# Kernel optimization log

Measured on AMD Instinct MI355X. Metric: run time of the kernel, lower is better.

## Reference

```python
import jax, jax.numpy as jnp
import numpy as np

NUM_RBF = 16
K_NB = 30
N_LAYERS = 4
N_HEADS = 4
HID = 64

def _ln(x, g, b, eps=1e-5):
    m = jnp.mean(x, -1, keepdims=True)
    v = jnp.mean((x - m) ** 2, -1, keepdims=True)
    return (x - m) / jnp.sqrt(v + eps) * g + b

def _edges(coords, mask):
    # KNN graph from Calpha coords; RBF-embed neighbor distances.
    mask2d = mask[:, :, None] * mask[:, None, :]                      # [B,L,L]
    dX = coords[:, :, None, :] - coords[:, None, :, :]
    D = jnp.sqrt(jnp.sum(dX * dX, -1) + 1e-6)                         # [B,L,L]
    D_max = jnp.max(D, -1, keepdims=True)
    D_adj = D + (1.0 - mask2d) * D_max                                # push padded pairs far away
    negD, E_idx = jax.lax.top_k(-D_adj, K_NB)                         # k smallest distances
    D_nb = -negD                                                      # [B,L,K]
    mu = jnp.linspace(2.0, 22.0, NUM_RBF)
    sigma = (22.0 - 2.0) / NUM_RBF
    rbf = jnp.exp(-(((D_nb[..., None] - mu) / sigma) ** 2))           # [B,L,K,16]
    return rbf, E_idx

def _gather(h, idx):
    # h [B,L,C], idx [B,L,K] -> [B,L,K,C]
    return jax.vmap(lambda hb, ib: hb[ib])(h, idx)

def setup_inputs() -> dict:
    key = jax.random.key(0)
    ks = iter(jax.random.split(key, 40))
    B, L, F = 8, 2048, 1038
    def w(shape, fan_in):
        return jax.random.normal(next(ks), shape, jnp.float32) / np.sqrt(fan_in)
    return {
        "coords": jax.random.normal(next(ks), (B, L, 3), jnp.float32) * 10.0,
        "node_features": jax.random.normal(next(ks), (B, L, F), jnp.float32),
        "mask": jnp.ones((B, L), jnp.float32),
        "W_node": w((F, HID), F), "b_node": jnp.zeros((HID,), jnp.float32),
        "W_ee": w((NUM_RBF, NUM_RBF), NUM_RBF),
        "g_eln": jnp.ones((NUM_RBF,), jnp.float32), "b_eln": jnp.zeros((NUM_RBF,), jnp.float32),
        "W_ep": w((NUM_RBF, HID), NUM_RBF), "b_ep": jnp.zeros((HID,), jnp.float32),
        "WQ": w((N_LAYERS, HID, HID), HID), "bQ": jnp.zeros((N_LAYERS, HID), jnp.float32),
        "WK": w((N_LAYERS, 2 * HID, HID), 2 * HID), "bK": jnp.zeros((N_LAYERS, HID), jnp.float32),
        "WV": w((N_LAYERS, 2 * HID, HID), 2 * HID), "bV": jnp.zeros((N_LAYERS, HID), jnp.float32),
        "WO": w((N_LAYERS, HID, HID), HID), "bO": jnp.zeros((N_LAYERS, HID), jnp.float32),
        "g1": jnp.ones((N_LAYERS, HID), jnp.float32), "b1": jnp.zeros((N_LAYERS, HID), jnp.float32),
        "W1": w((N_LAYERS, HID, 4 * HID), HID), "bf1": jnp.zeros((N_LAYERS, 4 * HID), jnp.float32),
        "W2": w((N_LAYERS, 4 * HID, HID), 4 * HID), "bf2": jnp.zeros((N_LAYERS, HID), jnp.float32),
        "g2": jnp.ones((N_LAYERS, HID), jnp.float32), "b2": jnp.zeros((N_LAYERS, HID), jnp.float32),
        "W_out": w((HID, 1), HID), "b_out": jnp.zeros((1,), jnp.float32),
    }

def reference(coords, node_features, mask, W_node, b_node, W_ee, g_eln, b_eln,
              W_ep, b_ep, WQ, bQ, WK, bK, WV, bV, WO, bO, g1, b1,
              W1, bf1, W2, bf2, g2, b2, W_out, b_out):
    B, L = mask.shape
    d = HID // N_HEADS
    rbf, E_idx = _edges(coords, mask)
    E = _ln(rbf @ W_ee, g_eln, b_eln)                                 # EdgeFeatures embedding+norm
    h_E = E @ W_ep + b_ep                                             # [B,L,K,HID]
    h_V = node_features @ W_node + b_node                             # [B,L,HID]
    mask_attend = _gather(mask[..., None], E_idx)[..., 0] * mask[..., None]  # [B,L,K]
    for l in range(N_LAYERS):
        h_EV = jnp.concatenate([h_E, _gather(h_V, E_idx)], -1)        # [B,L,K,2*HID]
        Q = (h_V @ WQ[l] + bQ[l]).reshape(B, L, N_HEADS, d)
        Kt = (h_EV @ WK[l] + bK[l]).reshape(B, L, K_NB, N_HEADS, d)
        V = (h_EV @ WV[l] + bV[l]).reshape(B, L, K_NB, N_HEADS, d)
        logits = jnp.einsum('blhd,blkhd->blhk', Q, Kt) / np.sqrt(d).astype(np.float32)
        m = mask_attend[:, :, None, :]                                # [B,L,1,K]
        logits = jnp.where(m > 0, logits, jnp.finfo(logits.dtype).min)
        attend = jax.nn.softmax(logits, -1) * m
        upd = jnp.einsum('blhk,blkhd->blhd', attend, V).reshape(B, L, HID)
        dh = upd @ WO[l] + bO[l]
        h_V = _ln(h_V + dh, g1[l], b1[l])
        ffn = jax.nn.relu(h_V @ W1[l] + bf1[l]) @ W2[l] + bf2[l]
        h_V = _ln(h_V + ffn, g2[l], b2[l])
        h_V = h_V * mask[..., None]
    logits_out = (h_V @ W_out + b_out)[..., 0]                        # [B,L]
    return logits_out
```

## Files before the change

### kernel.cpp

```cpp
#include <hip/hip_runtime.h>
#include <hip/hip_fp16.h>

#define L_ 2048
#define NROW 16384
#define FIN 1038

__global__ __launch_bounds__(256) void k_node_part(const float* __restrict__ X,
                                                   const float* __restrict__ W,
                                                   float* __restrict__ Part) {
  const int rb = blockIdx.x >> 2;
  const int split = blockIdx.x & 3;
  const int kStart = split * 260;
  const int kEnd = (split == 3) ? FIN : (kStart + 260);
  const int t = threadIdx.x;
  const int row0 = rb * 128;
  __shared__ float Xs[2][16][132];
  __shared__ float Ws[2][16][64];
  const int ri = t >> 3;
  const int ci = t & 7;
  const int sxr = t >> 2;
  const int sxk = (t & 3) * 4;
  const int swr = t >> 4;
  const int swc = (t & 15) * 4;

// ... 131 lines not shown
  float dmax = 0.f;
#pragma unroll
  for (int u = 0; u < 8; u++) {
    int j = t + 256 * u;
    float dx = cix - cb[j * 3 + 0];
    float dy = ciy - cb[j * 3 + 1];
    float dz = ciz - cb[j * 3 + 2];
    float dist = sqrtf(dx * dx + dy * dy + dz * dz + 1e-6f);
    d[u] = dist;
    mj[u] = mb[j];
    dmax = fmaxf(dmax, dist);
  }
#pragma unroll
  for (int off = 32; off; off >>= 1) dmax = fmaxf(dmax, __shfl_xor(dmax, off, 64));
  if (lane == 0) sredf[wid] = dmax;
#pragma unroll
  for (int q = 0; q < 8; q++) hist[t * 8 + q] = 0u;
  __syncthreads();
  dmax = fmaxf(fmaxf(sredf[0], sredf[1]), fmaxf(sredf[2], sredf[3]));
  const float scale = 1024.0f / fmaxf(dmax, 1e-20f);
  float adj[8];
  int bin[8];
#pragma unroll
  for (int u = 0; u < 8; u++) {
    adj[u] = d[u] + (1.f - mi * mj[u]) * dmax;
    int bi = (int)(adj[u] * scale);
    bin[u] = bi < 2047 ? bi : 2047;
    atomicAdd(&hist[bin[u]], 1u);
  }
  __syncthreads();
  unsigned int c[8];
  unsigned int local = 0;
#pragma unroll
  for (int q = 0; q < 8; q++) { c[q] = hist[t * 8 + q]; local += c[q]; }
  unsigned int incl = local;
#pragma unroll
  for (int off = 1; off < 64; off <<= 1) {
    unsigned int v = __shfl_up(incl, off, 64);
    if (lane >= off) incl += v;
  }
  if (lane == 63) wtot[wid] = incl;
  __syncthreads();
  unsigned int excl = incl - local;
  for (int w = 0; w < wid; w++) excl += wtot[w];
  if (excl < 30u && excl + local >= 30u) {
    unsigned int run = excl;
#pragma unroll
    for (int q = 0; q < 8; q++) {
      if (run + c[q] >= 30u) { s_bin = t * 8 + q; s_need = 30 - (int)run; break; }
      run += c[q];
    }
  }
  __syncthreads();
  const int tbin = s_bin;
  int pos[8];
#pragma unroll
  for (int u = 0; u < 8; u++) {
    pos[u] = -1;
    if (bin[u] == tbin) {
      int p = atomicAdd(&s_lcnt, 1);
      if (p < 64) { s_lkey[p] = __float_as_uint(adj[u]); s_lidx[p] = t + 256 * u; pos[u] = p; }
    }
  }
  __syncthreads();
  {
    int n = s_lcnt < 64 ? s_lcnt : 64;
    if (t < n) {
      unsigned int k0 = s_lkey[t];
      int j0 = s_lidx[t];
      int r = 0;
      for (int m = 0; m < n; m++) {
        unsigned int km = s_lkey[m];
        r += (km < k0) || (km == k0 && s_lidx[m] < j0);
      }
      s_sel[t] = (r < s_need) ? 1 : 0;
    }
  }
  __syncthreads();
#pragma unroll
  for (int u = 0; u < 8; u++) {
    bool sel = (bin[u] < tbin) || (pos[u] >= 0 && s_sel[pos[u]]);
    if (sel) {
      int o = atomicAdd(&s_outcnt, 1);
      if (o < 30) { sJ[o] = t + 256 * u; sD[o] = adj[u]; }
    }
  }
  __syncthreads();
  if (t < 30) Eidx[(size_t)row * 30 + t] = sJ[t];
  for (int o = t; o < 480; o += 256) {
    int k = o >> 4, s = o & 15;
    float mu = 2.0f + (4.0f / 3.0f) * (float)s;
    float z = (sD[k] - mu) * 0.8f;
    sRBF[k][s] = __expf(-z * z);
  }
  __syncthreads();
  if (t < 240) {
    int k = t >> 3, p = t & 7;
    int c0 = p * 2, c1 = c0 + 1;
    float e0 = 0.f, e1 = 0.f;
#pragma unroll
    for (int s = 0; s < 16; s++) {
      float r = sRBF[k][s];
      e0 += r * sWee[s][c0];
      e1 += r * sWee[s][c1];
    }
    float s1 = e0 + e1, s2 = e0 * e0 + e1 * e1;
#pragma unroll
    for (int m = 1; m < 8; m <<= 1) {
      s1 += __shfl_xor(s1, m, 64);
      s2 += __shfl_xor(s2, m, 64);
    }
    float mean = s1 * (1.f / 16.f);
    float var = s2 * (1.f / 16.f) - mean * mean;
    float inv = rsqrtf(var + 1e-5f);
    Eln[(size_t)row * 480 + k * 16 + c0] = __float2half((e0 - mean) * inv * sg[c0] + sb[c0]);
    Eln[(size_t)row * 480 + k * 16 + c1] = __float2half((e1 - mean) * inv * sg[c1] + sb[c1]);
  }
}

__global__ __launch_bounds__(256) void k_prep(const float* __restrict__ Wep,
                                              const float* __restrict__ bep,
                                              const float* __restrict__ WK,
                                              const float* __restrict__ bK,
                                              const float* __restrict__ WV,
                                              const float* __restrict__ bV,
                                              float* __restrict__ WKfold,
                                              float* __restrict__ bK2,
                                              float* __restrict__ WepWV,
                                              float* __restrict__ bV2) {
  const int l = blockIdx.x >> 1, isV = blockIdx.x & 1;
  const float* W = (isV ? WV : WK) + (size_t)l * 8192;
  const float* bsrc = (isV ? bV : bK) + l * 64;
  float* fold = (isV ? WepWV : WKfold) + l * 1024;
  float* b2 = (isV ? bV2 : bK2) + l * 64;
  __shared__ float sW[64][64];
  __shared__ float sWep[16][64];
  const int t = threadIdx.x;
  for (int q = 0; q < 16; q++) { int i = t + 256 * q; sW[i >> 6][i & 63] = W[i]; }
  for (int q = 0; q < 4; q++)  { int i = t + 256 * q; sWep[i >> 6][i & 63] = Wep[i]; }
  __syncthreads();
  const int c = t & 63, rg = t >> 6;
  for (int r = rg; r < 16; r += 4) {
    float a = 0.f;
    for (int s = 0; s < 64; s++) a += sWep[r][s] * sW[s][c];
    fold[r * 64 + c] = a;
  }
  if (t < 64) {
    float a = bsrc[t];
    for (int s = 0; s < 64; s++) a += bep[s] * sW[s][t];
    b2[t] = a;
  }
}

__global__ __launch_bounds__(256) void k_gemm64(const float* __restrict__ X,
                                                const float* __restrict__ W,
                                                const float* __restrict__ bias,
                                                float* __restrict__ out) {
  __shared__ float Xs[64][64];
  __shared__ float Ws[64][64];
  const int t = threadIdx.x;
  const int row0 = blockIdx.x * 64;
#pragma unroll
  for (int q = 0; q < 16; q++) {
    int i = t + 256 * q;
    int r = i >> 6, c = i & 63;
    Xs[r][c] = X[(size_t)(row0 + r) * 64 + c];
    Ws[r][c] = W[i];
  }
  __syncthreads();
  const int c = t & 63, rg = t >> 6;
  float acc[16];
#pragma unroll
  for (int u = 0; u < 16; u++) acc[u] = 0.f;
#pragma unroll
  for (int s0 = 0; s0 < 64; s0 += 4) {
    float w0 = Ws[s0][c], w1 = Ws[s0 + 1][c], w2 = Ws[s0 + 2][c], w3 = Ws[s0 + 3][c];
#pragma unroll
    for (int u = 0; u < 16; u++) {
      const float4 a = *(const float4*)&Xs[rg + 4 * u][s0];
      acc[u] += a.x * w0 + a.y * w1 + a.z * w2 + a.w * w3;
    }
  }
  const float bb = bias[c];
#pragma unroll
  for (int u = 0; u < 16; u++)
    out[(size_t)(row0 + rg + 4 * u) * 64 + c] = acc[u] + bb;
}

__global__ __launch_bounds__(256) void k_qw(const float* __restrict__ Q,
                                            const float* __restrict__ WK,
                                            const float* __restrict__ WKfold,
                                            const float* __restrict__ bK2,
                                            float* __restrict__ QWn,
                                            float* __restrict__ eqw,
                                            float* __restrict__ qb2) {
  __shared__ float sQ[64 * 68];
  __shared__ float sb[64];
  const int t = threadIdx.x;
  const int row0 = blockIdx.x * 64;
  for (int q = 0; q < 16; q++) {
    int i = t + 256 * q;
    int r = i >> 6, c = i & 63;
    sQ[r * 68 + c] = Q[(size_t)(row0 + r) * 64 + c];
  }
  if (t < 64) sb[t] = bK2[t];
  const int h = t >> 6, s2 = t & 63;
  const float4 wk0 = *(const float4*)&WK[(size_t)(64 + s2) * 64 + h * 16 + 0];
  const float4 wk1 = *(const float4*)&WK[(size_t)(64 + s2) * 64 + h * 16 + 4];
  const float4 wk2 = *(const float4*)&WK[(size_t)(64 + s2) * 64 + h * 16 + 8];
  const float4 wk3 = *(const float4*)&WK[(size_t)(64 + s2) * 64 + h * 16 + 12];
  __syncthreads();
  for (int r = 0; r < 64; r++) {
    const float4 q0 = *(const float4*)&sQ[r * 68 + h * 16 + 0];
    const float4 q1 = *(const float4*)&sQ[r * 68 + h * 16 + 4];
    const float4 q2 = *(const float4*)&sQ[r * 68 + h * 16 + 8];
    const float4 q3 = *(const float4*)&sQ[r * 68 + h * 16 + 12];
    float a = q0.x * wk0.x + q0.y * wk0.y + q0.z * wk0.z + q0.w * wk0.w
            + q1.x * wk1.x + q1.y * wk1.y + q1.z * wk1.z + q1.w * wk1.w
            + q2.x * wk2.x + q2.y * wk2.y + q2.z * wk2.z + q2.w * wk2.w
            + q3.x * wk3.x + q3.y * wk3.y + q3.z * wk3.z + q3.w * wk3.w;
    QWn[(size_t)(row0 + r) * 256 + h * 64 + s2] = a;
  }
  {
    const int hh = t >> 6, rb4 = (t >> 4) & 3, tt = t & 15;
    const float4 wf0 = *(const float4*)&WKfold[tt * 64 + hh * 16 + 0];
    const float4 wf1 = *(const float4*)&WKfold[tt * 64 + hh * 16 + 4];
    const float4 wf2 = *(const float4*)&WKfold[tt * 64 + hh * 16 + 8];
    const float4 wf3 = *(const float4*)&WKfold[tt * 64 + hh * 16 + 12];
    for (int rr = 0; rr < 16; rr++) {
      const int r = rr * 4 + rb4;
      const float4 q0 = *(const float4*)&sQ[r * 68 + hh * 16 + 0];
      const float4 q1 = *(const float4*)&sQ[r * 68 + hh * 16 + 4];
      const float4 q2 = *(const float4*)&sQ[r * 68 + hh * 16 + 8];
      const float4 q3 = *(const float4*)&sQ[r * 68 + hh * 16 + 12];
      float a = q0.x * wf0.x + q0.y * wf0.y + q0.z * wf0.z + q0.w * wf0.w
              + q1.x * wf1.x + q1.y * wf1.y + q1.z * wf1.z + q1.w * wf1.w
              + q2.x * wf2.x + q2.y * wf2.y + q2.z * wf2.z + q2.w * wf2.w
              + q3.x * wf3.x + q3.y * wf3.y + q3.z * wf3.z + q3.w * wf3.w;
      eqw[(size_t)(row0 + r) * 64 + hh * 16 + tt] = a;
    }
  }
  {
    const int r = t >> 2, h2 = t & 3;
    float a = 0.f;
#pragma unroll
    for (int d = 0; d < 16; d++) a += sQ[r * 68 + h2 * 16 + d] * sb[h2 * 16 + d];
    qb2[(size_t)(row0 + r) * 4 + h2] = a;
  }
}

__global__ __launch_bounds__(256) void k_attn(
    const __half* __restrict__ Eln, const int* __restrict__ Eidx,
    const float* __restrict__ hV, const float* __restrict__ mask,
    const float* __restrict__ QWn, const float* __restrict__ eqw,
    const float* __restrict__ qb2,
    float* __restrict__ Pg, float* __restrict__ attsum) {
  const int row = blockIdx.x;
  const int b = row >> 11;
  const int t = threadIdx.x;
  const int lane = t & 63, wid = t >> 6;
  __shared__ float sHV[30 * 65];
  __shared__ float sE[30 * 17];
  __shared__ float sQn[256];
  __shared__ float swq[64];
  __shared__ float sqb2[4];
  __shared__ float smk[32];

  sQn[t] = QWn[(size_t)row * 256 + t];
  if (t < 64) swq[t] = eqw[(size_t)row * 64 + t];
  if (t < 4) sqb2[t] = qb2[(size_t)row * 4 + t];
  if (t < 30) smk[t] = mask[(b << 11) + Eidx[(size_t)row * 30 + t]] * mask[row];
  for (int o = t; o < 480; o += 256)
    sE[(o >> 4) * 17 + (o & 15)] = __half2float(Eln[(size_t)row * 480 + o]);
#pragma unroll
  for (int q = 0; q < 8; q++) {
    int o = t + 256 * q;
    if (o < 1920) {
      int k = o >> 6, c = o & 63;
      int j = Eidx[(size_t)row * 30 + k];
      sHV[k * 65 + c] = hV[((size_t)(b << 11) + j) * 64 + c];
    }
  }
  __syncthreads();

  const int kk = (lane < 30) ? lane : (lane - 30);
  const int sbase = (lane < 30) ? 0 : 32;
  const int tbase = (lane < 30) ? 0 : 8;
  float lg = 0.f;
  if (lane < 60) {
#pragma unroll
    for (int s = 0; s < 32; s++)
      lg += sHV[kk * 65 + sbase + s] * sQn[wid * 64 + sbase + s];
#pragma unroll
    for (int tt = 0; tt < 8; tt++)
      lg += sE[kk * 17 + tbase + tt] * swq[wid * 16 + tbase + tt];
  }
  float oth = __shfl(lg, lane + 30, 64);
  float mk = (lane < 30) ? smk[lane] : 0.f;
  float lgv = (lane < 30 && mk > 0.f) ? (lg + oth + sqb2[wid]) * 0.25f
                                      : -3.402823466e38f;
  float mx = lgv;
#pragma unroll
  for (int off = 32; off; off >>= 1) mx = fmaxf(mx, __shfl_xor(mx, off, 64));
  float e = (lane < 30) ? __expf(lgv - mx) : 0.f;
  float den = e;
#pragma unroll
  for (int off = 32; off; off >>= 1) den += __shfl_xor(den, off, 64);
  float att = e * (1.f / den) * mk;
  float ss = att;
#pragma unroll
  for (int off = 32; off; off >>= 1) ss += __shfl_xor(ss, off, 64);
  float pn = 0.f, ea = 0.f;
  for (int k2 = 0; k2 < 30; k2++) {
    float a = __shfl(att, k2, 64);
    pn += a * sHV[k2 * 65 + lane];
    float ev = sE[k2 * 17 + (lane & 15)];
    if (lane < 16) ea += a * ev;
  }
  float* pr = Pg + (size_t)row * 320 + wid * 80;
  pr[lane] = pn;
  if (lane < 16) pr[64 + lane] = ea;
  if (lane == 0) attsum[(size_t)row * 4 + wid] = ss;
}

__global__ __launch_bounds__(256) void k_upd(const float* __restrict__ Pg,
                                             const float* __restrict__ ats,
                                             const float* __restrict__ WV,
                                             const float* __restrict__ WepWV,
                                             const float* __restrict__ bV2,
                                             float* __restrict__ U) {
  __shared__ float sWVb[64 * 64];
  __shared__ float sWf[16 * 64];
  __shared__ float sb[64];
  __shared__ float sP[8 * 320];
  const int t = threadIdx.x;
  const int row0 = blockIdx.x * 8;
  for (int q = 0; q < 16; q++) {
    int i = t + 256 * q;
    sWVb[i] = WV[4096 + i];
  }
  for (int q = 0; q < 4; q++) {
    int i = t + 256 * q;
    sWf[i] = WepWV[i];
  }
  if (t < 64) sb[t] = bV2[t];
  for (int q = 0; q < 10; q++) {
    int i = t + 256 * q;
    sP[i] = Pg[(size_t)row0 * 320 + i];
  }
  __syncthreads();
  const int c = t & 63, rg = t >> 6;
  const int h = c >> 4;
  const int r0 = rg * 2;
  float a0 = 0.f, a1 = 0.f;
#pragma unroll 8
  for (int s = 0; s < 64; s++) {
    float w = sWVb[s * 64 + c];
    a0 += sP[r0 * 320 + h * 80 + s] * w;
    a1 += sP[(r0 + 1) * 320 + h * 80 + s] * w;
  }
#pragma unroll
  for (int tt = 0; tt < 16; tt++) {
    float w = sWf[tt * 64 + c];
    a0 += sP[r0 * 320 + h * 80 + 64 + tt] * w;
    a1 += sP[(r0 + 1) * 320 + h * 80 + 64 + tt] * w;
  }
  const float bv = sb[c];
  const int grow = row0 + r0;
  U[(size_t)grow * 64 + c] = a0 + ats[(size_t)grow * 4 + h] * bv;
  U[(size_t)(grow + 1) * 64 + c] = a1 + ats[(size_t)(grow + 1) * 4 + h] * bv;
}

__global__ __launch_bounds__(256) void k_resln(const float* __restrict__ U,
                                               const float* __restrict__ WO,
                                               const float* __restrict__ bO,
                                               const float* __restrict__ g,
                                               const float* __restrict__ bb,
                                               float* __restrict__ hV) {
  __shared__ float sUt[64][16];
  __shared__ float sW[64][64];
  __shared__ float sO[16][64];
  const int t = threadIdx.x;
  const int row0 = blockIdx.x * 16;
#pragma unroll
  for (int q = 0; q < 4; q++) {
    int i = t + 256 * q;
    int r = i >> 6, cc = i & 63;
    sUt[cc][r] = U[(size_t)(row0 + r) * 64 + cc];
  }
#pragma unroll
  for (int q = 0; q < 16; q++) {
    int i = t + 256 * q;
    sW[i >> 6][i & 63] = WO[i];
  }
  __syncthreads();
  const int c = t & 63, rg = t >> 6;
  float acc[4] = {0.f, 0.f, 0.f, 0.f};
#pragma unroll
  for (int s = 0; s < 64; s++) {
    float w = sW[s][c];
    const float4 x = *(const float4*)&sUt[s][rg * 4];
    acc[0] += x.x * w; acc[1] += x.y * w; acc[2] += x.z * w; acc[3] += x.w * w;
  }
  const float bv = bO[c];
#pragma unroll
  for (int u = 0; u < 4; u++) sO[rg * 4 + u][c] = acc[u] + bv;
  __syncthreads();
  const int lane = t & 63, wv = t >> 6;
  const float gv = g[lane], bbv = bb[lane];
  for (int r = wv; r < 16; r += 4) {
    const int row = row0 + r;
    float x = hV[(size_t)row * 64 + lane] + sO[r][lane];
    float s1 = x, s2 = x * x;
#pragma unroll
    for (int off = 32; off; off >>= 1) {
      s1 += __shfl_xor(s1, off, 64);
      s2 += __shfl_xor(s2, off, 64);
    }
    float m = s1 * (1.f / 64.f);
    float var = s2 * (1.f / 64.f) - m * m;
    float inv = rsqrtf(var + 1e-5f);
    hV[(size_t)row * 64 + lane] = (x - m) * inv * gv + bbv;
  }
}

__global__ __launch_bounds__(256) void k_ffn1(const float* __restrict__ X,
                                              const float* __restrict__ W1,
                                              const float* __restrict__ bf1,
                                              float* __restrict__ T) {
  __shared__ float sXt[64][16];
  __shared__ float sW[32][256];
  const int t = threadIdx.x;
  const int row0 = blockIdx.x * 16;
#pragma unroll
  for (int q = 0; q < 4; q++) {
    int i = t + 256 * q;
    int r = i >> 6, cc = i & 63;
    sXt[cc][r] = X[(size_t)(row0 + r) * 64 + cc];
  }
  float acc[16];
#pragma unroll
  for (int u = 0; u < 16; u++) acc[u] = 0.f;
  for (int kc = 0; kc < 64; kc += 32) {
    __syncthreads();
#pragma unroll
    for (int q = 0; q < 32; q++) {
      int i = t + 256 * q;
      sW[i >> 8][i & 255] = W1[(size_t)(kc + (i >> 8)) * 256 + (i & 255)];
    }
    __syncthreads();
#pragma unroll
    for (int s = 0; s < 32; s++) {
      float w = sW[s][t];
      const float4 x0 = *(const float4*)&sXt[kc + s][0];
      const float4 x1 = *(const float4*)&sXt[kc + s][4];
      const float4 x2 = *(const float4*)&sXt[kc + s][8];
      const float4 x3 = *(const float4*)&sXt[kc + s][12];
      acc[0] += x0.x * w; acc[1] += x0.y * w; acc[2] += x0.z * w; acc[3] += x0.w * w;
      acc[4] += x1.x * w; acc[5] += x1.y * w; acc[6] += x1.z * w; acc[7] += x1.w * w;
      acc[8] += x2.x * w; acc[9] += x2.y * w; acc[10] += x2.z * w; acc[11] += x2.w * w;
      acc[12] += x3.x * w; acc[13] += x3.y * w; acc[14] += x3.z * w; acc[15] += x3.w * w;
    }
  }
  const float bv = bf1[t];
#pragma unroll
  for (int r = 0; r < 16; r++)
    T[(size_t)(row0 + r) * 256 + t] = fmaxf(acc[r] + bv, 0.f);
}

__global__ __launch_bounds__(256) void k_ffn2(const float* __restrict__ T,
                                              const float* __restrict__ W2,
                                              const float* __restrict__ bf2,
                                              const float* __restrict__ g,
                                              const float* __restrict__ bb,
                                              const float* __restrict__ mask,
                                              float* __restrict__ hV) {
  __shared__ float sTt[64][16];
  __shared__ float sW[64][64];
  __shared__ float sO[16][64];
  const int t = threadIdx.x;
  const int row0 = blockIdx.x * 16;
  const int c = t & 63, rg = t >> 6;
  float acc[4] = {0.f, 0.f, 0.f, 0.f};
  for (int kc = 0; kc < 256; kc += 64) {
    __syncthreads();
#pragma unroll
    for (int q = 0; q < 4; q++) {
      int i = t + 256 * q;
      int r = i >> 6, cc = i & 63;
      sTt[cc][r] = T[(size_t)(row0 + r) * 256 + kc + cc];
    }
#pragma unroll
    for (int q = 0; q < 16; q++) {
      int i = t + 256 * q;
      sW[i >> 6][i & 63] = W2[(size_t)(kc + (i >> 6)) * 64 + (i & 63)];
    }
    __syncthreads();
#pragma unroll
    for (int s = 0; s < 64; s++) {
      float w = sW[s][c];
      const float4 x = *(const float4*)&sTt[s][rg * 4];
      acc[0] += x.x * w; acc[1] += x.y * w; acc[2] += x.z * w; acc[3] += x.w * w;
    }
  }
  const float bv = bf2[c];
#pragma unroll
  for (int u = 0; u < 4; u++) sO[rg * 4 + u][c] = acc[u] + bv;
  __syncthreads();
  const int lane = t & 63, wv = t >> 6;
  const float gv = g[lane], bbv = bb[lane];
  for (int r = wv; r < 16; r += 4) {
    const int row = row0 + r;
    float x = hV[(size_t)row * 64 + lane] + sO[r][lane];
    float s1 = x, s2 = x * x;
#pragma unroll
    for (int off = 32; off; off >>= 1) {
      s1 += __shfl_xor(s1, off, 64);
      s2 += __shfl_xor(s2, off, 64);
    }
    float m = s1 * (1.f / 64.f);
    float var = s2 * (1.f / 64.f) - m * m;
    float inv = rsqrtf(var + 1e-5f);
    float y = (x - m) * inv * gv + bbv;
    hV[(size_t)row * 64 + lane] = y * mask[row];
  }
}

__global__ __launch_bounds__(256) void k_out(const float* __restrict__ hV,
                                             const float* __restrict__ Wo,
                                             const float* __restrict__ bo,
                                             float* __restrict__ out) {
  const int t = threadIdx.x;
  const int lane = t & 63, wv = t >> 6;
  const int row = blockIdx.x * 4 + wv;
  float v = hV[(size_t)row * 64 + lane] * Wo[lane];
#pragma unroll
  for (int off = 32; off; off >>= 1) v += __shfl_xor(v, off, 64);
  if (lane == 0) out[row] = v + bo[0];
}

extern "C" void kernel_launch(void* const* d_in, const int* in_sizes, int n_in,
                              void* d_out, int out_size, void* d_ws, size_t ws_size,
                              hipStream_t stream) {
  const float* coords = (const float*)d_in[0];
  const float* nodef = (const float*)d_in[1];
  const float* mask = (const float*)d_in[2];
  const float* W_node = (const float*)d_in[3];
  const float* b_node = (const float*)d_in[4];
  const float* W_ee = (const float*)d_in[5];
  const float* g_eln = (const float*)d_in[6];
  const float* b_eln = (const float*)d_in[7];
  const float* W_ep = (const float*)d_in[8];
  const float* b_ep = (const float*)d_in[9];
  const float* WQ = (const float*)d_in[10];
  const float* bQ = (const float*)d_in[11];
  const float* WK = (const float*)d_in[12];
  const float* bK = (const float*)d_in[13];
  const float* WV = (const float*)d_in[14];
  const float* bV = (const float*)d_in[15];
  const float* WO = (const float*)d_in[16];
  const float* bO = (const float*)d_in[17];
  const float* g1 = (const float*)d_in[18];
  const float* b1 = (const float*)d_in[19];
  const float* W1 = (const float*)d_in[20];
  const float* bf1 = (const float*)d_in[21];
  const float* W2 = (const float*)d_in[22];
  const float* bf2 = (const float*)d_in[23];
  const float* g2 = (const float*)d_in[24];
  const float* b2 = (const float*)d_in[25];
  const float* W_out = (const float*)d_in[26];
  const float* b_out = (const float*)d_in[27];

  float* ws = (float*)d_ws;
  float* hV = ws;
  float* Qb = hV + 1048576;
  float* QWn = Qb + 1048576;
  float* eqw = QWn + 4194304;
  float* Pg = eqw + 1048576;
  float* qb2 = Pg + 5242880;
  float* ats = qb2 + 65536;
  int* Eidx = (int*)(ats + 65536);
  __half* Eln = (__half*)(Eidx + 491520);
  float* WKfold = (float*)(Eln + 7864320);
  float* bK2 = WKfold + 4096;
  float* WepWV = bK2 + 256;
  float* bV2 = WepWV + 4096;
  float* Tb = QWn;
  float* Part = Pg;

  k_node_part<<<512, 256, 0, stream>>>(nodef, W_node, Part);
  k_node_sum<<<1024, 256, 0, stream>>>(Part, b_node, hV);
  k_edges<<<16384, 256, 0, stream>>>(coords, mask, W_ee, g_eln, b_eln, Eidx, Eln);
  k_prep<<<8, 256, 0, stream>>>(W_ep, b_ep, WK, bK, WV, bV, WKfold, bK2, WepWV, bV2);
  for (int l = 0; l < 4; l++) {
    k_gemm64<<<256, 256, 0, stream>>>(hV, WQ + l * 4096, bQ + l * 64, Qb);
    k_qw<<<256, 256, 0, stream>>>(Qb, WK + l * 8192, WKfold + l * 1024, bK2 + l * 64,
                                  QWn, eqw, qb2);
    k_attn<<<16384, 256, 0, stream>>>(Eln, Eidx, hV, mask, QWn, eqw, qb2, Pg, ats);
    k_upd<<<2048, 256, 0, stream>>>(Pg, ats, WV + l * 8192, WepWV + l * 1024,
                                    bV2 + l * 64, Qb);
    k_resln<<<1024, 256, 0, stream>>>(Qb, WO + l * 4096, bO + l * 64,
                                      g1 + l * 64, b1 + l * 64, hV);
    k_ffn1<<<1024, 256, 0, stream>>>(hV, W1 + l * 16384, bf1 + l * 256, Tb);
    k_ffn2<<<1024, 256, 0, stream>>>(Tb, W2 + l * 16384, bf2 + l * 64,
                                     g2 + l * 64, b2 + l * 64, mask, hV);
  }
  k_out<<<4096, 256, 0, stream>>>(hV, W_out, b_out, (float*)d_out);
}
```

Before: 903.5 us.

## Fold WQ into key projections and fuse update/LN and FFN kernels

```diff
diff --git a/kernel.cpp b/kernel.cpp
--- a/kernel.cpp
+++ b/kernel.cpp
@@ -307,108 +307,107 @@
   }
 }
 
-__global__ __launch_bounds__(256) void k_gemm64(const float* __restrict__ X,
-                                                const float* __restrict__ W,
-                                                const float* __restrict__ bias,
-                                                float* __restrict__ out) {
-  __shared__ float Xs[64][64];
+__global__ __launch_bounds__(256) void k_prep2(const float* __restrict__ WQ,
+                                               const float* __restrict__ bQ,
+                                               const float* __restrict__ WK,
+                                               const float* __restrict__ WKfold,
+                                               const float* __restrict__ bK2,
+                                               float* __restrict__ Wbig,
+                                               float* __restrict__ bbig) {
+  const int l = blockIdx.x;
+  const float* wq = WQ + (size_t)l * 4096;
+  const float* bq = bQ + l * 64;
+  const float* wkb = WK + (size_t)l * 8192 + 4096;
+  const float* wkf = WKfold + l * 1024;
+  const float* bk2 = bK2 + l * 64;
+  float* wb = Wbig + (size_t)l * (64 * 384);
+  float* bb = bbig + l * 384;
+  const int t = threadIdx.x;
+  for (int c = t; c < 384; c += 256) {
+    if (c >= 324) {
+      for (int j = 0; j < 64; j++) wb[j * 384 + c] = 0.f;
+      bb[c] = 0.f;
+      continue;
+    }
+    float v[16];
+    int h;
+    if (c < 256) {
+      h = c >> 6;
+      int s = c & 63;
+#pragma unroll
+      for (int d = 0; d < 16; d++) v[d] = wkb[s * 64 + h * 16 + d];
+    } else if (c < 320) {
+      int cc = c - 256;
+      h = cc >> 4;
+      int tt = cc & 15;
+#pragma unroll
+      for (int d = 0; d < 16; d++) v[d] = wkf[tt * 64 + h * 16 + d];
+    } else {
+      h = c - 320;
+#pragma unroll
+      for (int d = 0; d < 16; d++) v[d] = bk2[h * 16 + d];
+    }
+    float bacc = 0.f;
+#pragma unroll
+    for (int d = 0; d < 16; d++) bacc += bq[h * 16 + d] * v[d];
+    bb[c] = bacc;
+    for (int j = 0; j < 64; j++) {
+      float a = 0.f;
+#pragma unroll
+      for (int d = 0; d < 16; d++) a += wq[j * 64 + h * 16 + d] * v[d];
+      wb[j * 384 + c] = a;
+    }
+  }
+}
+
+__global__ __launch_bounds__(256) void k_qkv(const float* __restrict__ hV,
+                                             const float* __restrict__ Wbig,
+                                             const float* __restrict__ bbig,
+                                             float* __restrict__ QWall) {
+  __shared__ float Xs[32][64];
   __shared__ float Ws[64][64];
-  const int t = threadIdx.x;
-  const int row0 = blockIdx.x * 64;
-#pragma unroll
-  for (int q = 0; q < 16; q++) {
+  __shared__ float sbb[384];
+  const int t = threadIdx.x;
+  const int row0 = blockIdx.x * 32;
+#pragma unroll
+  for (int q = 0; q < 8; q++) {
     int i = t + 256 * q;
-    int r = i >> 6, c = i & 63;
-    Xs[r][c] = X[(size_t)(row0 + r) * 64 + c];
-    Ws[r][c] = W[i];
-  }
-  __syncthreads();
+    if (i < 2048) Xs[i >> 6][i & 63] = hV[(size_t)(row0 + (i >> 6)) * 64 + (i & 63)];
+  }
+  for (int i = t; i < 384; i += 256) sbb[i] = bbig[i];
   const int c = t & 63, rg = t >> 6;
-  float acc[16];
-#pragma unroll
-  for (int u = 0; u < 16; u++) acc[u] = 0.f;
-#pragma unroll
-  for (int s0 = 0; s0 < 64; s0 += 4) {
-    float w0 = Ws[s0][c], w1 = Ws[s0 + 1][c], w2 = Ws[s0 + 2][c], w3 = Ws[s0 + 3][c];
-#pragma unroll
-    for (int u = 0; u < 16; u++) {
-      const float4 a = *(const float4*)&Xs[rg + 4 * u][s0];
-      acc[u] += a.x * w0 + a.y * w1 + a.z * w2 + a.w * w3;
-    }
-  }
-  const float bb = bias[c];
-#pragma unroll
-  for (int u = 0; u < 16; u++)
-    out[(size_t)(row0 + rg + 4 * u) * 64 + c] = acc[u] + bb;
-}
-
-__global__ __launch_bounds__(256) void k_qw(const float* __restrict__ Q,
-                                            const float* __restrict__ WK,
-                                            const float* __restrict__ WKfold,
-                                            const float* __restrict__ bK2,
-                                            float* __restrict__ QWn,
-                                            float* __restrict__ eqw,
-                                            float* __restrict__ qb2) {
-  __shared__ float sQ[64 * 68];
-  __shared__ float sb[64];
-  const int t = threadIdx.x;
-  const int row0 = blockIdx.x * 64;
-  for (int q = 0; q < 16; q++) {
-    int i = t + 256 * q;
-    int r = i >> 6, c = i & 63;
-    sQ[r * 68 + c] = Q[(size_t)(row0 + r) * 64 + c];
-  }
-  if (t < 64) sb[t] = bK2[t];
-  const int h = t >> 6, s2 = t & 63;
-  const float4 wk0 = *(const float4*)&WK[(size_t)(64 + s2) * 64 + h * 16 + 0];
-  const float4 wk1 = *(const float4*)&WK[(size_t)(64 + s2) * 64 + h * 16 + 4];
-  const float4 wk2 = *(const float4*)&WK[(size_t)(64 + s2) * 64 + h * 16 + 8];
-  const float4 wk3 = *(const float4*)&WK[(size_t)(64 + s2) * 64 + h * 16 + 12];
-  __syncthreads();
-  for (int r = 0; r < 64; r++) {
-    const float4 q0 = *(const float4*)&sQ[r * 68 + h * 16 + 0];
-    const float4 q1 = *(const float4*)&sQ[r * 68 + h * 16 + 4];
-    const float4 q2 = *(const float4*)&sQ[r * 68 + h * 16 + 8];
-    const float4 q3 = *(const float4*)&sQ[r * 68 + h * 16 + 12];
-    float a = q0.x * wk0.x + q0.y * wk0.y + q0.z * wk0.z + q0.w * wk0.w
-            + q1.x * wk1.x + q1.y * wk1.y + q1.z * wk1.z + q1.w * wk1.w
-            + q2.x * wk2.x + q2.y * wk2.y + q2.z * wk2.z + q2.w * wk2.w
-            + q3.x * wk3.x + q3.y * wk3.y + q3.z * wk3.z + q3.w * wk3.w;
-    QWn[(size_t)(row0 + r) * 256 + h * 64 + s2] = a;
-  }
-  {
-    const int hh = t >> 6, rb4 = (t >> 4) & 3, tt = t & 15;
-    const float4 wf0 = *(const float4*)&WKfold[tt * 64 + hh * 16 + 0];
-    const float4 wf1 = *(const float4*)&WKfold[tt * 64 + hh * 16 + 4];
-    const float4 wf2 = *(const float4*)&WKfold[tt * 64 + hh * 16 + 8];
-    const float4 wf3 = *(const float4*)&WKfold[tt * 64 + hh * 16 + 12];
-    for (int rr = 0; rr < 16; rr++) {
-      const int r = rr * 4 + rb4;
-      const float4 q0 = *(const float4*)&sQ[r * 68 + hh * 16 + 0];
-      const float4 q1 = *(const float4*)&sQ[r * 68 + hh * 16 + 4];
-      const float4 q2 = *(const float4*)&sQ[r * 68 + hh * 16 + 8];
-      const float4 q3 = *(const float4*)&sQ[r * 68 + hh * 16 + 12];
-      float a = q0.x * wf0.x + q0.y * wf0.y + q0.z * wf0.z + q0.w * wf0.w
-              + q1.x * wf1.x + q1.y * wf1.y + q1.z * wf1.z + q1.w * wf1.w
-              + q2.x * wf2.x + q2.y * wf2.y + q2.z * wf2.z + q2.w * wf2.w
-              + q3.x * wf3.x + q3.y * wf3.y + q3.z * wf3.z + q3.w * wf3.w;
-      eqw[(size_t)(row0 + r) * 64 + hh * 16 + tt] = a;
-    }
-  }
-  {
-    const int r = t >> 2, h2 = t & 3;
-    float a = 0.f;
-#pragma unroll
-    for (int d = 0; d < 16; d++) a += sQ[r * 68 + h2 * 16 + d] * sb[h2 * 16 + d];
-    qb2[(size_t)(row0 + r) * 4 + h2] = a;
+  for (int ch = 0; ch < 6; ch++) {
+    __syncthreads();
+#pragma unroll
+    for (int q = 0; q < 16; q++) {
+      int i = t + 256 * q;
+      int k = i >> 6, cc = i & 63;
+      Ws[k][cc] = Wbig[(size_t)k * 384 + ch * 64 + cc];
+    }
+    __syncthreads();
+    float acc[8];
+#pragma unroll
+    for (int u = 0; u < 8; u++) acc[u] = 0.f;
+#pragma unroll
+    for (int s0 = 0; s0 < 64; s0 += 4) {
+      float w0 = Ws[s0][c], w1 = Ws[s0 + 1][c], w2 = Ws[s0 + 2][c], w3 = Ws[s0 + 3][c];
+#pragma unroll
+      for (int u = 0; u < 8; u++) {
+        const float4 a = *(const float4*)&Xs[rg * 8 + u][s0];
+        acc[u] += a.x * w0 + a.y * w1 + a.z * w2 + a.w * w3;
+      }
+    }
+    const float bv = sbb[ch * 64 + c];
+#pragma unroll
+    for (int u = 0; u < 8; u++)
+      QWall[(size_t)(row0 + rg * 8 + u) * 384 + ch * 64 + c] = acc[u] + bv;
   }
 }
 
 __global__ __launch_bounds__(256) void k_attn(
     const __half* __restrict__ Eln, const int* __restrict__ Eidx,
     const float* __restrict__ hV, const float* __restrict__ mask,
-    const float* __restrict__ QWn, const float* __restrict__ eqw,
-    const float* __restrict__ qb2,
+    const float* __restrict__ QWall,
     float* __restrict__ Pg, float* __restrict__ attsum) {
   const int row = blockIdx.x;
   const int b = row >> 11;
@@ -421,9 +420,9 @@
   __shared__ float sqb2[4];
   __shared__ float smk[32];
 
-  sQn[t] = QWn[(size_t)row * 256 + t];
-  if (t < 64) swq[t] = eqw[(size_t)row * 64 + t];
-  if (t < 4) sqb2[t] = qb2[(size_t)row * 4 + t];
+  sQn[t] = QWall[(size_t)row * 384 + t];
+  if (t < 64) swq[t] = QWall[(size_t)row * 384 + 256 + t];
+  if (t < 4) sqb2[t] = QWall[(size_t)row * 384 + 320 + t];
   if (t < 30) smk[t] = mask[(b << 11) + Eidx[(size_t)row * 30 + t]] * mask[row];
   for (int o = t; o < 480; o += 256)
     sE[(o >> 4) * 17 + (o & 15)] = __half2float(Eln[(size_t)row * 480 + o]);
@@ -478,94 +477,141 @@
   if (lane == 0) attsum[(size_t)row * 4 + wid] = ss;
 }
 
-__global__ __launch_bounds__(256) void k_upd(const float* __restrict__ Pg,
-                                             const float* __restrict__ ats,
-                                             const float* __restrict__ WV,
-                                             const float* __restrict__ WepWV,
-                                             const float* __restrict__ bV2,
-                                             float* __restrict__ U) {
-  __shared__ float sWVb[64 * 64];
-  __shared__ float sWf[16 * 64];
-  __shared__ float sb[64];
-  __shared__ float sP[8 * 320];
-  const int t = threadIdx.x;
-  const int row0 = blockIdx.x * 8;
-  for (int q = 0; q < 16; q++) {
-    int i = t + 256 * q;
-    sWVb[i] = WV[4096 + i];
-  }
-  for (int q = 0; q < 4; q++) {
-    int i = t + 256 * q;
-    sWf[i] = WepWV[i];
-  }
-  if (t < 64) sb[t] = bV2[t];
-  for (int q = 0; q < 10; q++) {
-    int i = t + 256 * q;
-    sP[i] = Pg[(size_t)row0 * 320 + i];
-  }
-  __syncthreads();
-  const int c = t & 63, rg = t >> 6;
-  const int h = c >> 4;
-  const int r0 = rg * 2;
-  float a0 = 0.f, a1 = 0.f;
-#pragma unroll 8
-  for (int s = 0; s < 64; s++) {
-    float w = sWVb[s * 64 + c];
-    a0 += sP[r0 * 320 + h * 80 + s] * w;
-    a1 += sP[(r0 + 1) * 320 + h * 80 + s] * w;
-  }
-#pragma unroll
-  for (int tt = 0; tt < 16; tt++) {
-    float w = sWf[tt * 64 + c];
-    a0 += sP[r0 * 320 + h * 80 + 64 + tt] * w;
-    a1 += sP[(r0 + 1) * 320 + h * 80 + 64 + tt] * w;
-  }
-  const float bv = sb[c];
-  const int grow = row0 + r0;
-  U[(size_t)grow * 64 + c] = a0 + ats[(size_t)grow * 4 + h] * bv;
-  U[(size_t)(grow + 1) * 64 + c] = a1 + ats[(size_t)(grow + 1) * 4 + h] * bv;
-}
-
-__global__ __launch_bounds__(256) void k_resln(const float* __restrict__ U,
+__global__ __launch_bounds__(256) void k_updln(const float* __restrict__ Pg,
+                                               const float* __restrict__ ats,
+                                               const float* __restrict__ WV,
+                                               const float* __restrict__ WepWV,
+                                               const float* __restrict__ bV2,
                                                const float* __restrict__ WO,
                                                const float* __restrict__ bO,
                                                const float* __restrict__ g,
-                                               const float* __restrict__ bb,
+                                               const float* __restrict__ bb_,
                                                float* __restrict__ hV) {
-  __shared__ float sUt[64][16];
-  __shared__ float sW[64][64];
-  __shared__ float sO[16][64];
+  __shared__ float sWVb[4096];
+  __shared__ float sWf[1024];
+  __shared__ float sWO[4096];
+  __shared__ float sP[16 * 320];
+  __shared__ float sU[16 * 68];
+  __shared__ float sbV2[64], sbO[64], sg[64], sbb[64], sats[64];
+  const int t = threadIdx.x;
+  const int row0 = blockIdx.x * 16;
+#pragma unroll
+  for (int q = 0; q < 16; q++) { int i = t + 256 * q; sWVb[i] = WV[4096 + i]; }
+#pragma unroll
+  for (int q = 0; q < 4; q++) { int i = t + 256 * q; sWf[i] = WepWV[i]; }
+#pragma unroll
+  for (int q = 0; q < 16; q++) { int i = t + 256 * q; sWO[i] = WO[i]; }
+#pragma unroll
+  for (int q = 0; q < 20; q++) { int i = t + 256 * q; sP[i] = Pg[(size_t)row0 * 320 + i]; }
+  if (t < 64) {
+    sbV2[t] = bV2[t];
+    sbO[t] = bO[t];
+    sg[t] = g[t];
+    sbb[t] = bb_[t];
+    sats[t] = ats[(size_t)row0 * 4 + t];
+  }
+  __syncthreads();
+  const int c = t & 63, rg = t >> 6;
+  const int h = c >> 4;
+#pragma unroll
+  for (int ui = 0; ui < 4; ui++) {
+    const int r = rg * 4 + ui;
+    float a = sats[r * 4 + h] * sbV2[c];
+#pragma unroll 8
+    for (int s = 0; s < 64; s++) a += sP[r * 320 + h * 80 + s] * sWVb[s * 64 + c];
+#pragma unroll
+    for (int tt = 0; tt < 16; tt++) a += sP[r * 320 + h * 80 + 64 + tt] * sWf[tt * 64 + c];
+    sU[r * 68 + c] = a;
+  }
+  __syncthreads();
+  const int j = c;
+#pragma unroll
+  for (int ui = 0; ui < 4; ui++) {
+    const int r = rg * 4 + ui;
+    float a = sbO[j];
+#pragma unroll 8
+    for (int cc = 0; cc < 64; cc++) a += sU[r * 68 + cc] * sWO[cc * 64 + j];
+    float x = hV[(size_t)(row0 + r) * 64 + j] + a;
+    float s1 = x, s2 = x * x;
+#pragma unroll
+    for (int off = 32; off; off >>= 1) {
+      s1 += __shfl_xor(s1, off, 64);
+      s2 += __shfl_xor(s2, off, 64);
+    }
+    float m = s1 * (1.f / 64.f);
+    float var = s2 * (1.f / 64.f) - m * m;
+    float inv = rsqrtf(var + 1e-5f);
+    hV[(size_t)(row0 + r) * 64 + j] = (x - m) * inv * sg[j] + sbb[j];
+  }
+}
+
+__global__ __launch_bounds__(256) void k_ffn(const float* __restrict__ hVin,
+                                             const float* __restrict__ W1,
+                                             const float* __restrict__ bf1,
+                                             const float* __restrict__ W2,
+                                             const float* __restrict__ bf2,
+                                             const float* __restrict__ g,
+                                             const float* __restrict__ bb_,
+                                             const float* __restrict__ mask,
+                                             float* __restrict__ hV) {
+  __shared__ float sX[16 * 68];
+  __shared__ float sW1[32 * 256];
+  __shared__ float sT[16 * 260];
+  __shared__ float sW2[64 * 64];
+  __shared__ float sbf1[256], sbf2[64], sg[64], sbb[64];
   const int t = threadIdx.x;
   const int row0 = blockIdx.x * 16;
 #pragma unroll
   for (int q = 0; q < 4; q++) {
     int i = t + 256 * q;
     int r = i >> 6, cc = i & 63;
-    sUt[cc][r] = U[(size_t)(row0 + r) * 64 + cc];
-  }
-#pragma unroll
-  for (int q = 0; q < 16; q++) {
-    int i = t + 256 * q;
-    sW[i >> 6][i & 63] = WO[i];
-  }
-  __syncthreads();
-  const int c = t & 63, rg = t >> 6;
-  float acc[4] = {0.f, 0.f, 0.f, 0.f};
-#pragma unroll
-  for (int s = 0; s < 64; s++) {
-    float w = sW[s][c];
-    const float4 x = *(const float4*)&sUt[s][rg * 4];
-    acc[0] += x.x * w; acc[1] += x.y * w; acc[2] += x.z * w; acc[3] += x.w * w;
-  }
-  const float bv = bO[c];
-#pragma unroll
-  for (int u = 0; u < 4; u++) sO[rg * 4 + u][c] = acc[u] + bv;
-  __syncthreads();
-  const int lane = t & 63, wv = t >> 6;
-  const float gv = g[lane], bbv = bb[lane];
-  for (int r = wv; r < 16; r += 4) {
-    const int row = row0 + r;
-    float x = hV[(size_t)row * 64 + lane] + sO[r][lane];
+    sX[r * 68 + cc] = hVin[(size_t)(row0 + r) * 64 + cc];
+  }
+  sbf1[t] = bf1[t];
+  if (t < 64) { sbf2[t] = bf2[t]; sg[t] = g[t]; sbb[t] = bb_[t]; }
+  float accT[16];
+#pragma unroll
+  for (int u = 0; u < 16; u++) accT[u] = 0.f;
+  for (int ch = 0; ch < 2; ch++) {
+    __syncthreads();
+#pragma unroll
+    for (int q = 0; q < 32; q++) {
+      int i = t + 256 * q;
+      sW1[i] = W1[(size_t)ch * 8192 + i];
+    }
+    __syncthreads();
+#pragma unroll
+    for (int s = 0; s < 32; s++) {
+      const float w = sW1[s * 256 + t];
+#pragma unroll
+      for (int r = 0; r < 16; r++) accT[r] += sX[r * 68 + ch * 32 + s] * w;
+    }
+  }
+  __syncthreads();
+#pragma unroll
+  for (int r = 0; r < 16; r++) sT[r * 260 + t] = fmaxf(accT[r] + sbf1[t], 0.f);
+  const int j = t & 63, rg = t >> 6;
+  float acc2[4] = {0.f, 0.f, 0.f, 0.f};
+  for (int ch2 = 0; ch2 < 4; ch2++) {
+    __syncthreads();
+#pragma unroll
+    for (int q = 0; q < 16; q++) {
+      int i = t + 256 * q;
+      sW2[i] = W2[(size_t)ch2 * 4096 + i];
+    }
+    __syncthreads();
+#pragma unroll 8
+    for (int s = 0; s < 64; s++) {
+      const float w = sW2[s * 64 + j];
+#pragma unroll
+      for (int u = 0; u < 4; u++)
+        acc2[u] += sT[(rg * 4 + u) * 260 + ch2 * 64 + s] * w;
+    }
+  }
+#pragma unroll
+  for (int u = 0; u < 4; u++) {
+    const int r = rg * 4 + u;
+    float x = hVin[(size_t)(row0 + r) * 64 + j] + acc2[u] + sbf2[j];
     float s1 = x, s2 = x * x;
 #pragma unroll
     for (int off = 32; off; off >>= 1) {
@@ -575,109 +621,8 @@
     float m = s1 * (1.f / 64.f);
     float var = s2 * (1.f / 64.f) - m * m;
     float inv = rsqrtf(var + 1e-5f);
-    hV[(size_t)row * 64 + lane] = (x - m) * inv * gv + bbv;
-  }
-}
-
-__global__ __launch_bounds__(256) void k_ffn1(const float* __restrict__ X,
-                                              const float* __restrict__ W1,
-                                              const float* __restrict__ bf1,
-                                              float* __restrict__ T) {
-  __shared__ float sXt[64][16];
-  __shared__ float sW[32][256];
-  const int t = threadIdx.x;
-  const int row0 = blockIdx.x * 16;
-#pragma unroll
-  for (int q = 0; q < 4; q++) {
-    int i = t + 256 * q;
-    int r = i >> 6, cc = i & 63;
-    sXt[cc][r] = X[(size_t)(row0 + r) * 64 + cc];
-  }
-  float acc[16];
-#pragma unroll
-  for (int u = 0; u < 16; u++) acc[u] = 0.f;
-  for (int kc = 0; kc < 64; kc += 32) {
-    __syncthreads();
-#pragma unroll
-    for (int q = 0; q < 32; q++) {
-      int i = t + 256 * q;
-      sW[i >> 8][i & 255] = W1[(size_t)(kc + (i >> 8)) * 256 + (i & 255)];
-    }
-    __syncthreads();
-#pragma unroll
-    for (int s = 0; s < 32; s++) {
-      float w = sW[s][t];
-      const float4 x0 = *(const float4*)&sXt[kc + s][0];
-      const float4 x1 = *(const float4*)&sXt[kc + s][4];
-      const float4 x2 = *(const float4*)&sXt[kc + s][8];
-      const float4 x3 = *(const float4*)&sXt[kc + s][12];
-      acc[0] += x0.x * w; acc[1] += x0.y * w; acc[2] += x0.z * w; acc[3] += x0.w * w;
-      acc[4] += x1.x * w; acc[5] += x1.y * w; acc[6] += x1.z * w; acc[7] += x1.w * w;
-      acc[8] += x2.x * w; acc[9] += x2.y * w; acc[10] += x2.z * w; acc[11] += x2.w * w;
-      acc[12] += x3.x * w; acc[13] += x3.y * w; acc[14] += x3.z * w; acc[15] += x3.w * w;
-    }
-  }
-  const float bv = bf1[t];
-#pragma unroll
-  for (int r = 0; r < 16; r++)
-    T[(size_t)(row0 + r) * 256 + t] = fmaxf(acc[r] + bv, 0.f);
-}
-
-__global__ __launch_bounds__(256) void k_ffn2(const float* __restrict__ T,
-                                              const float* __restrict__ W2,
-                                              const float* __restrict__ bf2,
-                                              const float* __restrict__ g,
-                                              const float* __restrict__ bb,
-                                              const float* __restrict__ mask,
-                                              float* __restrict__ hV) {
-  __shared__ float sTt[64][16];
-  __shared__ float sW[64][64];
-  __shared__ float sO[16][64];
-  const int t = threadIdx.x;
-  const int row0 = blockIdx.x * 16;
-  const int c = t & 63, rg = t >> 6;
-  float acc[4] = {0.f, 0.f, 0.f, 0.f};
-  for (int kc = 0; kc < 256; kc += 64) {
-    __syncthreads();
-#pragma unroll
-    for (int q = 0; q < 4; q++) {
-      int i = t + 256 * q;
-      int r = i >> 6, cc = i & 63;
-      sTt[cc][r] = T[(size_t)(row0 + r) * 256 + kc + cc];
-    }
-#pragma unroll
-    for (int q = 0; q < 16; q++) {
-      int i = t + 256 * q;
-      sW[i >> 6][i & 63] = W2[(size_t)(kc + (i >> 6)) * 64 + (i & 63)];
-    }
-    __syncthreads();
-#pragma unroll
-    for (int s = 0; s < 64; s++) {
-      float w = sW[s][c];
-      const float4 x = *(const float4*)&sTt[s][rg * 4];
-      acc[0] += x.x * w; acc[1] += x.y * w; acc[2] += x.z * w; acc[3] += x.w * w;
-    }
-  }
-  const float bv = bf2[c];
-#pragma unroll
-  for (int u = 0; u < 4; u++) sO[rg * 4 + u][c] = acc[u] + bv;
-  __syncthreads();
-  const int lane = t & 63, wv = t >> 6;
-  const float gv = g[lane], bbv = bb[lane];
-  for (int r = wv; r < 16; r += 4) {
-    const int row = row0 + r;
-    float x = hV[(size_t)row * 64 + lane] + sO[r][lane];
-    float s1 = x, s2 = x * x;
-#pragma unroll
-    for (int off = 32; off; off >>= 1) {
-      s1 += __shfl_xor(s1, off, 64);
-      s2 += __shfl_xor(s2, off, 64);
-    }
-    float m = s1 * (1.f / 64.f);
-    float var = s2 * (1.f / 64.f) - m * m;
-    float inv = rsqrtf(var + 1e-5f);
-    float y = (x - m) * inv * gv + bbv;
-    hV[(size_t)row * 64 + lane] = y * mask[row];
+    float y = (x - m) * inv * sg[j] + sbb[j];
+    hV[(size_t)(row0 + r) * 64 + j] = y * mask[row0 + r];
   }
 }
 
@@ -728,37 +673,34 @@
 
   float* ws = (float*)d_ws;
   float* hV = ws;
-  float* Qb = hV + 1048576;
-  float* QWn = Qb + 1048576;
-  float* eqw = QWn + 4194304;
-  float* Pg = eqw + 1048576;
-  float* qb2 = Pg + 5242880;
-  float* ats = qb2 + 65536;
+  float* QWall = hV + 1048576;
+  float* Pg = QWall + 6291456;
+  float* ats = Pg + 5242880;
   int* Eidx = (int*)(ats + 65536);
   __half* Eln = (__half*)(Eidx + 491520);
   float* WKfold = (float*)(Eln + 7864320);
   float* bK2 = WKfold + 4096;
   float* WepWV = bK2 + 256;
   float* bV2 = WepWV + 4096;
-  float* Tb = QWn;
-  float* Part = Pg;
+  float* Wbig = bV2 + 256;
+  float* bbig = Wbig + 98304;
+  float* Part = QWall;
 
   k_node_part<<<512, 256, 0, stream>>>(nodef, W_node, Part);
   k_node_sum<<<1024, 256, 0, stream>>>(Part, b_node, hV);
   k_edges<<<16384, 256, 0, stream>>>(coords, mask, W_ee, g_eln, b_eln, Eidx, Eln);
   k_prep<<<8, 256, 0, stream>>>(W_ep, b_ep, WK, bK, WV, bV, WKfold, bK2, WepWV, bV2);
+  k_prep2<<<4, 256, 0, stream>>>(WQ, bQ, WK, WKfold, bK2, Wbig, bbig);
   for (int l = 0; l < 4; l++) {
-    k_gemm64<<<256, 256, 0, stream>>>(hV, WQ + l * 4096, bQ + l * 64, Qb);
-    k_qw<<<256, 256, 0, stream>>>(Qb, WK + l * 8192, WKfold + l * 1024, bK2 + l * 64,
-                                  QWn, eqw, qb2);
-    k_attn<<<16384, 256, 0, stream>>>(Eln, Eidx, hV, mask, QWn, eqw, qb2, Pg, ats);
-    k_upd<<<2048, 256, 0, stream>>>(Pg, ats, WV + l * 8192, WepWV + l * 1024,
-                                    bV2 + l * 64, Qb);
-    k_resln<<<1024, 256, 0, stream>>>(Qb, WO + l * 4096, bO + l * 64,
+    k_qkv<<<512, 256, 0, stream>>>(hV, Wbig + (size_t)l * 24576, bbig + l * 384, QWall);
+    k_attn<<<16384, 256, 0, stream>>>(Eln, Eidx, hV, mask, QWall, Pg, ats);
+    k_updln<<<1024, 256, 0, stream>>>(Pg, ats, WV + (size_t)l * 8192,
+                                      WepWV + l * 1024, bV2 + l * 64,
+                                      WO + (size_t)l * 4096, bO + l * 64,
                                       g1 + l * 64, b1 + l * 64, hV);
-    k_ffn1<<<1024, 256, 0, stream>>>(hV, W1 + l * 16384, bf1 + l * 256, Tb);
-    k_ffn2<<<1024, 256, 0, stream>>>(Tb, W2 + l * 16384, bf2 + l * 64,
-                                     g2 + l * 64, b2 + l * 64, mask, hV);
+    k_ffn<<<1024, 256, 0, stream>>>(hV, W1 + (size_t)l * 16384, bf1 + l * 256,
+                                    W2 + (size_t)l * 16384, bf2 + l * 64,
+                                    g2 + l * 64, b2 + l * 64, mask, hV);
   }
   k_out<<<4096, 256, 0, stream>>>(hV, W_out, b_out, (float*)d_out);
 }
```

Result: slower. 1.162 ms (+28.6%).

## Process eight rows per attention block with register-staged double buffering

Applied to the files above, without the earlier changes.

```diff
diff --git a/kernel.cpp b/kernel.cpp
--- a/kernel.cpp
+++ b/kernel.cpp
@@ -410,72 +410,113 @@
     const float* __restrict__ QWn, const float* __restrict__ eqw,
     const float* __restrict__ qb2,
     float* __restrict__ Pg, float* __restrict__ attsum) {
-  const int row = blockIdx.x;
-  const int b = row >> 11;
   const int t = threadIdx.x;
   const int lane = t & 63, wid = t >> 6;
-  __shared__ float sHV[30 * 65];
-  __shared__ float sE[30 * 17];
-  __shared__ float sQn[256];
-  __shared__ float swq[64];
-  __shared__ float sqb2[4];
-  __shared__ float smk[32];
-
-  sQn[t] = QWn[(size_t)row * 256 + t];
-  if (t < 64) swq[t] = eqw[(size_t)row * 64 + t];
-  if (t < 4) sqb2[t] = qb2[(size_t)row * 4 + t];
-  if (t < 30) smk[t] = mask[(b << 11) + Eidx[(size_t)row * 30 + t]] * mask[row];
-  for (int o = t; o < 480; o += 256)
-    sE[(o >> 4) * 17 + (o & 15)] = __half2float(Eln[(size_t)row * 480 + o]);
-#pragma unroll
-  for (int q = 0; q < 8; q++) {
-    int o = t + 256 * q;
-    if (o < 1920) {
-      int k = o >> 6, c = o & 63;
-      int j = Eidx[(size_t)row * 30 + k];
-      sHV[k * 65 + c] = hV[((size_t)(b << 11) + j) * 64 + c];
-    }
-  }
-  __syncthreads();
-
-  const int kk = (lane < 30) ? lane : (lane - 30);
-  const int sbase = (lane < 30) ? 0 : 32;
-  const int tbase = (lane < 30) ? 0 : 8;
-  float lg = 0.f;
-  if (lane < 60) {
-#pragma unroll
-    for (int s = 0; s < 32; s++)
-      lg += sHV[kk * 65 + sbase + s] * sQn[wid * 64 + sbase + s];
-#pragma unroll
-    for (int tt = 0; tt < 8; tt++)
-      lg += sE[kk * 17 + tbase + tt] * swq[wid * 16 + tbase + tt];
-  }
-  float oth = __shfl(lg, lane + 30, 64);
-  float mk = (lane < 30) ? smk[lane] : 0.f;
-  float lgv = (lane < 30 && mk > 0.f) ? (lg + oth + sqb2[wid]) * 0.25f
-                                      : -3.402823466e38f;
-  float mx = lgv;
-#pragma unroll
-  for (int off = 32; off; off >>= 1) mx = fmaxf(mx, __shfl_xor(mx, off, 64));
-  float e = (lane < 30) ? __expf(lgv - mx) : 0.f;
-  float den = e;
-#pragma unroll
-  for (int off = 32; off; off >>= 1) den += __shfl_xor(den, off, 64);
-  float att = e * (1.f / den) * mk;
-  float ss = att;
-#pragma unroll
-  for (int off = 32; off; off >>= 1) ss += __shfl_xor(ss, off, 64);
-  float pn = 0.f, ea = 0.f;
-  for (int k2 = 0; k2 < 30; k2++) {
-    float a = __shfl(att, k2, 64);
-    pn += a * sHV[k2 * 65 + lane];
-    float ev = sE[k2 * 17 + (lane & 15)];
-    if (lane < 16) ea += a * ev;
-  }
-  float* pr = Pg + (size_t)row * 320 + wid * 80;
-  pr[lane] = pn;
-  if (lane < 16) pr[64 + lane] = ea;
-  if (lane == 0) attsum[(size_t)row * 4 + wid] = ss;
+  __shared__ float sHV[2][30 * 65];
+  __shared__ float sE[2][30 * 17];
+  __shared__ float sQn[2][256];
+  __shared__ float swq[2][68];
+  __shared__ float smk[2][32];
+  const int row0 = blockIdx.x * 8;
+
+  float r_hv[8], r_e0, r_e1, r_q, r_w, r_mk;
+
+#define STAGE_LOAD(row)                                                       \
+  {                                                                           \
+    const int b2 = (row) >> 11;                                               \
+    r_q = QWn[(size_t)(row) * 256 + t];                                       \
+    r_w = (t < 64) ? eqw[(size_t)(row) * 64 + t]                              \
+                   : ((t < 68) ? qb2[(size_t)(row) * 4 + (t - 64)] : 0.f);    \
+    r_mk = (t < 30)                                                           \
+        ? mask[(b2 << 11) + Eidx[(size_t)(row) * 30 + t]] * mask[row]         \
+        : 0.f;                                                                \
+    r_e0 = __half2float(Eln[(size_t)(row) * 480 + t]);                        \
+    r_e1 = (t < 224) ? __half2float(Eln[(size_t)(row) * 480 + 256 + t]) : 0.f;\
+    _Pragma("unroll")                                                         \
+    for (int q = 0; q < 8; q++) {                                             \
+      int o = t + 256 * q;                                                    \
+      if (o < 1920) {                                                         \
+        int k = o >> 6, c = o & 63;                                           \
+        int j = Eidx[(size_t)(row) * 30 + k];                                 \
+        r_hv[q] = hV[((size_t)(b2 << 11) + j) * 64 + c];                      \
+      }                                                                       \
+    }                                                                         \
+  }
+
+#define STAGE_STORE(bf)                                                       \
+  {                                                                           \
+    sQn[bf][t] = r_q;                                                         \
+    if (t < 68) swq[bf][t] = r_w;                                             \
+    if (t < 30) smk[bf][t] = r_mk;                                            \
+    sE[bf][(t >> 4) * 17 + (t & 15)] = r_e0;                                  \
+    if (t < 224) {                                                            \
+      int o = t + 256;                                                        \
+      sE[bf][(o >> 4) * 17 + (o & 15)] = r_e1;                                \
+    }                                                                         \
+    _Pragma("unroll")                                                         \
+    for (int q = 0; q < 8; q++) {                                             \
+      int o = t + 256 * q;                                                    \
+      if (o < 1920) sHV[bf][(o >> 6) * 65 + (o & 63)] = r_hv[q];              \
+    }                                                                         \
+  }
+
+#define COMPUTE(bf, row)                                                      \
+  {                                                                           \
+    const int kk = (lane < 30) ? lane : (lane - 30);                          \
+    const int sbase = (lane < 30) ? 0 : 32;                                   \
+    const int tbase = (lane < 30) ? 0 : 8;                                    \
+    float lg = 0.f;                                                           \
+    if (lane < 60) {                                                          \
+      _Pragma("unroll")                                                       \
+      for (int s = 0; s < 32; s++)                                            \
+        lg += sHV[bf][kk * 65 + sbase + s] * sQn[bf][wid * 64 + sbase + s];   \
+      _Pragma("unroll")                                                       \
+      for (int tt = 0; tt < 8; tt++)                                          \
+        lg += sE[bf][kk * 17 + tbase + tt] * swq[bf][wid * 16 + tbase + tt];  \
+    }                                                                         \
+    float oth = __shfl(lg, lane + 30, 64);                                    \
+    float mk = (lane < 30) ? smk[bf][lane] : 0.f;                             \
+    float lgv = (lane < 30 && mk > 0.f)                                       \
+        ? (lg + oth + swq[bf][64 + wid]) * 0.25f : -3.402823466e38f;          \
+    float mx = lgv;                                                           \
+    _Pragma("unroll")                                                         \
+    for (int off = 32; off; off >>= 1) mx = fmaxf(mx, __shfl_xor(mx, off, 64)); \
+    float e = (lane < 30) ? __expf(lgv - mx) : 0.f;                           \
+    float den = e;                                                            \
+    _Pragma("unroll")                                                         \
+    for (int off = 32; off; off >>= 1) den += __shfl_xor(den, off, 64);       \
+    float att = e * (1.f / den) * mk;                                         \
+    float ss = att;                                                           \
+    _Pragma("unroll")                                                         \
+    for (int off = 32; off; off >>= 1) ss += __shfl_xor(ss, off, 64);         \
+    float pn = 0.f, ea = 0.f;                                                 \
+    for (int k2 = 0; k2 < 30; k2++) {                                         \
+      float a = __shfl(att, k2, 64);                                          \
+      pn += a * sHV[bf][k2 * 65 + lane];                                      \
+      float ev = sE[bf][k2 * 17 + (lane & 15)];                               \
+      if (lane < 16) ea += a * ev;                                            \
+    }                                                                         \
+    float* pr = Pg + (size_t)(row) * 320 + wid * 80;                          \
+    pr[lane] = pn;                                                            \
+    if (lane < 16) pr[64 + lane] = ea;                                        \
+    if (lane == 0) attsum[(size_t)(row) * 4 + wid] = ss;                      \
+  }
+
+  STAGE_LOAD(row0);
+  STAGE_STORE(0);
+  __syncthreads();
+  int bf = 0;
+#pragma unroll
+  for (int r = 0; r < 8; r++) {
+    if (r + 1 < 8) STAGE_LOAD(row0 + r + 1);
+    COMPUTE(bf, row0 + r);
+    if (r + 1 < 8) STAGE_STORE(bf ^ 1);
+    __syncthreads();
+    bf ^= 1;
+  }
+#undef STAGE_LOAD
+#undef STAGE_STORE
+#undef COMPUTE
 }
 
 __global__ __launch_bounds__(256) void k_upd(const float* __restrict__ Pg,
@@ -751,7 +792,7 @@
     k_gemm64<<<256, 256, 0, stream>>>(hV, WQ + l * 4096, bQ + l * 64, Qb);
     k_qw<<<256, 256, 0, stream>>>(Qb, WK + l * 8192, WKfold + l * 1024, bK2 + l * 64,
                                   QWn, eqw, qb2);
-    k_attn<<<16384, 256, 0, stream>>>(Eln, Eidx, hV, mask, QWn, eqw, qb2, Pg, ats);
+    k_attn<<<2048, 256, 0, stream>>>(Eln, Eidx, hV, mask, QWn, eqw, qb2, Pg, ats);
     k_upd<<<2048, 256, 0, stream>>>(Pg, ats, WV + l * 8192, WepWV + l * 1024,
                                     bV2 + l * 64, Qb);
     k_resln<<<1024, 256, 0, stream>>>(Qb, WO + l * 4096, bO + l * 64,
```

New measurement: 1.055 ms. 16.8% more time.
